# Kernel optimization log

Measured on AMD Instinct MI355X. Metric: run time of the kernel, lower is better.

## Reference

```python
import jax, jax.numpy as jnp
import numpy as np

B, T, L, D, K = 16, 2048, 1024, 512, 5  # batch, tokens, token_dim, d_model, kernel_size


def setup_inputs() -> dict:
    key = jax.random.key(0)
    k1, k2, k3 = jax.random.split(key, 3)
    x = jax.random.normal(k1, (B, T, L), dtype=jnp.float32)
    # Conv1d weight [d_model, in_ch=1, K] stored as [D, K]; torch default init ~ U(-1/sqrt(K), 1/sqrt(K))
    bound = 1.0 / np.sqrt(K)
    w = jax.random.uniform(k2, (D, K), dtype=jnp.float32, minval=-bound, maxval=bound)
    b = jax.random.uniform(k3, (D,), dtype=jnp.float32, minval=-bound, maxval=bound)
    return {"x": x, "w": w, "b": b}


def reference(x, w, b):
    # Faithful to: conv1d(in=1, out=D, k=K, padding=K//2) on each (b,t) row, then mean over length L.
    # Since mean-over-L is linear:
    #   out[b,t,d] = (1/L) * sum_l sum_k w[d,k] * x_pad[b,t,l+k] + bias[d]
    #             = (1/L) * sum_k w[d,k] * S[b,t,k],  S[b,t,k] = sum_{l=0}^{L-1} x_pad[b,t,l+k]
    # Computed exactly via cumsum of the zero-padded row; avoids the (B*T, D, L) conv tensor.
    Dm, Kk = w.shape
    Bb, Tt, Ll = x.shape
    p = Kk // 2
    xp = jnp.pad(x, ((0, 0), (0, 0), (p, p)))                 # [B, T, L+2p]
    c = jnp.cumsum(xp, axis=-1)                               # c[..., j] = sum of xp[..., :j+1]
    c = jnp.pad(c, ((0, 0), (0, 0), (1, 0)))                  # prefix sums, c[..., j] = sum of xp[..., :j]
    ks = jnp.arange(Kk)
    S = c[..., ks + Ll] - c[..., ks]                          # [B, T, K] windowed sums
    out = jnp.einsum('btk,dk->btd', S, w) / Ll + b            # [B, T, D]
    return out
```

## Files before the change

### kernel.cpp

```cpp
#include <hip/hip_runtime.h>

#define ROWS   (16 * 2048)
#define ROWLEN 1024
#define DMODEL 512


__global__ __launch_bounds__(256) void conv1d_token_encoder_kernel(
    const float* __restrict__ x,
    const float* __restrict__ w,
    const float* __restrict__ b,
    float* __restrict__ out)
{
    const int lane   = threadIdx.x & 63;
    const int wid    = blockIdx.x * (blockDim.x >> 6) + (threadIdx.x >> 6);
    const int nwaves = gridDim.x * (blockDim.x >> 6);
    const float invL = 1.0f / (float)ROWLEN;

    float cA[2][4], cm2[2][4], cm1[2][4], c0c[2][4], c1c[2][4], cb[2][4];
#pragma unroll
    for (int j = 0; j < 2; ++j) {
#pragma unroll
        for (int c = 0; c < 4; ++c) {
            const int d = 4 * lane + 256 * j + c;
            const float w0 = w[d * 5 + 0];
            const float w1 = w[d * 5 + 1];
            const float w2 = w[d * 5 + 2];
            const float w3 = w[d * 5 + 3];
            const float w4 = w[d * 5 + 4];
            cA[j][c]  = (w0 + w1 + w2 + w3 + w4) * invL;
            cm2[j][c] = w0 * invL;
            cm1[j][c] = (w0 + w1) * invL;
            c0c[j][c] = (w3 + w4) * invL;
            c1c[j][c] = w4 * invL;
            cb[j][c]  = b[d];
        }
    }

    for (int row = wid; row < ROWS; row += nwaves) {
        const float4* __restrict__ xr = (const float4*)(x + (size_t)row * ROWLEN);
        float4 v0 = xr[lane];
        float4 v1 = xr[lane + 64];
        float4 v2 = xr[lane + 128];
        float4 v3 = xr[lane + 192];

        float s = (v0.x + v0.y + v0.z + v0.w)
                + (v1.x + v1.y + v1.z + v1.w)
                + (v2.x + v2.y + v2.z + v2.w)
                + (v3.x + v3.y + v3.z + v3.w);
#pragma unroll
        for (int m = 1; m < 64; m <<= 1) s += __shfl_xor(s, m, 64);

        const float x0  = __shfl(v0.x, 0, 64);
        const float x1  = __shfl(v0.y, 0, 64);
        const float xm2 = __shfl(v3.z, 63, 64);
        const float xm1 = __shfl(v3.w, 63, 64);

        float4* __restrict__ orow = (float4*)(out + (size_t)row * DMODEL);
#pragma unroll
        for (int j = 0; j < 2; ++j) {
            float4 o;
            o.x = cA[j][0] * s - cm2[j][0] * xm2 - cm1[j][0] * xm1
                - c0c[j][0] * x0 - c1c[j][0] * x1 + cb[j][0];
            o.y = cA[j][1] * s - cm2[j][1] * xm2 - cm1[j][1] * xm1
                - c0c[j][1] * x0 - c1c[j][1] * x1 + cb[j][1];
            o.z = cA[j][2] * s - cm2[j][2] * xm2 - cm1[j][2] * xm1
                - c0c[j][2] * x0 - c1c[j][2] * x1 + cb[j][2];
            o.w = cA[j][3] * s - cm2[j][3] * xm2 - cm1[j][3] * xm1
                - c0c[j][3] * x0 - c1c[j][3] * x1 + cb[j][3];
            orow[lane + 64 * j] = o;
        }
    }
}

extern "C" void kernel_launch(void* const* d_in, const int* in_sizes, int n_in,
                              void* d_out, int out_size, void* d_ws, size_t ws_size,
                              hipStream_t stream) {
    const float* x = (const float*)d_in[0];
    const float* w = (const float*)d_in[1];
    const float* b = (const float*)d_in[2];
    float* out = (float*)d_out;

    conv1d_token_encoder_kernel<<<2048, 256, 0, stream>>>(x, w, b, out);
}
```

Measured before the change: 211.5 us.

## Process two rows per wave and stage weight coefficients through shared memory

Each wave now loads and reduces two rows per iteration, doubling the loads in flight to hide memory latency. Per-block coefficient setup is done cooperatively into LDS with coalesced weight reads instead of every lane reading strided weights from global memory. The grid is halved and launch bounds add a minimum-occupancy hint. Register pressure rises from holding two rows, and the kernel is bound by streaming x, so gains may be small.

```diff
diff --git a/kernel.cpp b/kernel.cpp
--- a/kernel.cpp
+++ b/kernel.cpp
@@ -5,69 +5,104 @@
 #define DMODEL 512
 
 
-__global__ __launch_bounds__(256) void conv1d_token_encoder_kernel(
+__global__ __launch_bounds__(256, 4) void conv1d_token_encoder_kernel(
     const float* __restrict__ x,
     const float* __restrict__ w,
     const float* __restrict__ b,
     float* __restrict__ out)
 {
-    const int lane   = threadIdx.x & 63;
-    const int wid    = blockIdx.x * (blockDim.x >> 6) + (threadIdx.x >> 6);
-    const int nwaves = gridDim.x * (blockDim.x >> 6);
+    __shared__ float cf[6][DMODEL];
+
+    const int tid    = threadIdx.x;
+    const int lane   = tid & 63;
+    const int wid    = blockIdx.x * 4 + (tid >> 6);
+    const int nwaves = gridDim.x * 4;
     const float invL = 1.0f / (float)ROWLEN;
 
-    float cA[2][4], cm2[2][4], cm1[2][4], c0c[2][4], c1c[2][4], cb[2][4];
+#pragma unroll
+    for (int g = 0; g < 2; ++g) {
+        const int d = tid + g * 256;
+        const float w0 = w[d * 5 + 0];
+        const float w1 = w[d * 5 + 1];
+        const float w2 = w[d * 5 + 2];
+        const float w3 = w[d * 5 + 3];
+        const float w4 = w[d * 5 + 4];
+        cf[0][d] = (w0 + w1 + w2 + w3 + w4) * invL;
+        cf[1][d] = w0 * invL;
+        cf[2][d] = (w0 + w1) * invL;
+        cf[3][d] = (w3 + w4) * invL;
+        cf[4][d] = w4 * invL;
+        cf[5][d] = b[d];
+    }
+    __syncthreads();
+
+    float4 A[2], M2[2], M1[2], C0[2], C1[2], Bb[2];
 #pragma unroll
     for (int j = 0; j < 2; ++j) {
-#pragma unroll
-        for (int c = 0; c < 4; ++c) {
-            const int d = 4 * lane + 256 * j + c;
-            const float w0 = w[d * 5 + 0];
-            const float w1 = w[d * 5 + 1];
-            const float w2 = w[d * 5 + 2];
-            const float w3 = w[d * 5 + 3];
-            const float w4 = w[d * 5 + 4];
-            cA[j][c]  = (w0 + w1 + w2 + w3 + w4) * invL;
-            cm2[j][c] = w0 * invL;
-            cm1[j][c] = (w0 + w1) * invL;
-            c0c[j][c] = (w3 + w4) * invL;
-            c1c[j][c] = w4 * invL;
-            cb[j][c]  = b[d];
-        }
+        const int d = 4 * lane + 256 * j;
+        A[j]  = *(const float4*)&cf[0][d];
+        M2[j] = *(const float4*)&cf[1][d];
+        M1[j] = *(const float4*)&cf[2][d];
+        C0[j] = *(const float4*)&cf[3][d];
+        C1[j] = *(const float4*)&cf[4][d];
+        Bb[j] = *(const float4*)&cf[5][d];
     }
 
-    for (int row = wid; row < ROWS; row += nwaves) {
-        const float4* __restrict__ xr = (const float4*)(x + (size_t)row * ROWLEN);
-        float4 v0 = xr[lane];
-        float4 v1 = xr[lane + 64];
-        float4 v2 = xr[lane + 128];
-        float4 v3 = xr[lane + 192];
+    for (int row = 2 * wid; row < ROWS; row += 2 * nwaves) {
+        const float4* __restrict__ xr0 = (const float4*)(x + (size_t)row * ROWLEN);
+        const float4* __restrict__ xr1 = (const float4*)(x + (size_t)(row + 1) * ROWLEN);
+        float4 a0 = xr0[lane];
+        float4 a1 = xr0[lane + 64];
+        float4 a2 = xr0[lane + 128];
+        float4 a3 = xr0[lane + 192];
+        float4 b0 = xr1[lane];
+        float4 b1 = xr1[lane + 64];
+        float4 b2 = xr1[lane + 128];
+        float4 b3 = xr1[lane + 192];
 
-        float s = (v0.x + v0.y + v0.z + v0.w)
-                + (v1.x + v1.y + v1.z + v1.w)
-                + (v2.x + v2.y + v2.z + v2.w)
-                + (v3.x + v3.y + v3.z + v3.w);
+        float s0 = (a0.x + a0.y + a0.z + a0.w) + (a1.x + a1.y + a1.z + a1.w)
+                 + (a2.x + a2.y + a2.z + a2.w) + (a3.x + a3.y + a3.z + a3.w);
+        float s1 = (b0.x + b0.y + b0.z + b0.w) + (b1.x + b1.y + b1.z + b1.w)
+                 + (b2.x + b2.y + b2.z + b2.w) + (b3.x + b3.y + b3.z + b3.w);
 #pragma unroll
-        for (int m = 1; m < 64; m <<= 1) s += __shfl_xor(s, m, 64);
+        for (int m = 1; m < 64; m <<= 1) {
+            s0 += __shfl_xor(s0, m, 64);
+            s1 += __shfl_xor(s1, m, 64);
+        }
 
-        const float x0  = __shfl(v0.x, 0, 64);
-        const float x1  = __shfl(v0.y, 0, 64);
-        const float xm2 = __shfl(v3.z, 63, 64);
-        const float xm1 = __shfl(v3.w, 63, 64);
+        const float x0_0  = __shfl(a0.x, 0, 64);
+        const float x1_0  = __shfl(a0.y, 0, 64);
+        const float xm2_0 = __shfl(a3.z, 63, 64);
+        const float xm1_0 = __shfl(a3.w, 63, 64);
+        const float x0_1  = __shfl(b0.x, 0, 64);
+        const float x1_1  = __shfl(b0.y, 0, 64);
+        const float xm2_1 = __shfl(b3.z, 63, 64);
+        const float xm1_1 = __shfl(b3.w, 63, 64);
 
-        float4* __restrict__ orow = (float4*)(out + (size_t)row * DMODEL);
+        float4* __restrict__ o0 = (float4*)(out + (size_t)row * DMODEL);
+        float4* __restrict__ o1 = (float4*)(out + (size_t)(row + 1) * DMODEL);
 #pragma unroll
         for (int j = 0; j < 2; ++j) {
-            float4 o;
-            o.x = cA[j][0] * s - cm2[j][0] * xm2 - cm1[j][0] * xm1
-                - c0c[j][0] * x0 - c1c[j][0] * x1 + cb[j][0];
-            o.y = cA[j][1] * s - cm2[j][1] * xm2 - cm1[j][1] * xm1
-                - c0c[j][1] * x0 - c1c[j][1] * x1 + cb[j][1];
-            o.z = cA[j][2] * s - cm2[j][2] * xm2 - cm1[j][2] * xm1
-                - c0c[j][2] * x0 - c1c[j][2] * x1 + cb[j][2];
-            o.w = cA[j][3] * s - cm2[j][3] * xm2 - cm1[j][3] * xm1
-                - c0c[j][3] * x0 - c1c[j][3] * x1 + cb[j][3];
-            orow[lane + 64 * j] = o;
+            float4 t;
+            t.x = A[j].x * s0 - M2[j].x * xm2_0 - M1[j].x * xm1_0
+                - C0[j].x * x0_0 - C1[j].x * x1_0 + Bb[j].x;
+            t.y = A[j].y * s0 - M2[j].y * xm2_0 - M1[j].y * xm1_0
+                - C0[j].y * x0_0 - C1[j].y * x1_0 + Bb[j].y;
+            t.z = A[j].z * s0 - M2[j].z * xm2_0 - M1[j].z * xm1_0
+                - C0[j].z * x0_0 - C1[j].z * x1_0 + Bb[j].z;
+            t.w = A[j].w * s0 - M2[j].w * xm2_0 - M1[j].w * xm1_0
+                - C0[j].w * x0_0 - C1[j].w * x1_0 + Bb[j].w;
+            o0[lane + 64 * j] = t;
+
+            t.x = A[j].x * s1 - M2[j].x * xm2_1 - M1[j].x * xm1_1
+                - C0[j].x * x0_1 - C1[j].x * x1_1 + Bb[j].x;
+            t.y = A[j].y * s1 - M2[j].y * xm2_1 - M1[j].y * xm1_1
+                - C0[j].y * x0_1 - C1[j].y * x1_1 + Bb[j].y;
+            t.z = A[j].z * s1 - M2[j].z * xm2_1 - M1[j].z * xm1_1
+                - C0[j].z * x0_1 - C1[j].z * x1_1 + Bb[j].z;
+            t.w = A[j].w * s1 - M2[j].w * xm2_1 - M1[j].w * xm1_1
+                - C0[j].w * x0_1 - C1[j].w * x1_1 + Bb[j].w;
+            o1[lane + 64 * j] = t;
         }
     }
 }
@@ -80,5 +115,5 @@
     const float* b = (const float*)d_in[2];
     float* out = (float*)d_out;
 
-    conv1d_token_encoder_kernel<<<2048, 256, 0, stream>>>(x, w, b, out);
+    conv1d_token_encoder_kernel<<<1024, 256, 0, stream>>>(x, w, b, out);
 }
```

New measurement: 214.0 us. About the same (+1.2%).
